# Kernel tuning notes

Hardware: AMD Instinct MI355X
Metric: run time of the kernel (lower is better)

The kernel has to match this reference:

```python
import jax, jax.numpy as jnp
import numpy as np

B, S, E, H, A = 2, 1024, 1024, 16, 3
HD = E // H

def setup_inputs() -> dict:
    key = jax.random.key(0)
    ks = jax.random.split(key, 8)
    return {
        "query": jax.random.normal(ks[0], (B, S, E), dtype=jnp.float32),
        "key": jax.random.normal(ks[1], (B, S, E), dtype=jnp.float32),
        "value": jax.random.normal(ks[2], (B, S, E), dtype=jnp.float32),
        "aid": jax.random.normal(ks[3], (B, S, S, A), dtype=jnp.float32),
        "mixer_w": jax.random.uniform(ks[4], (H, A + 1, 1), dtype=jnp.float32),
        "mixer_b": jax.random.uniform(ks[5], (H, 1), dtype=jnp.float32),
        "Wo": jax.random.normal(ks[6], (E, E), dtype=jnp.float32) * 0.02,
        "bo": jax.random.normal(ks[7], (E,), dtype=jnp.float32) * 0.02,
        "aid_scale": jnp.array([0.1], dtype=jnp.float32),
    }

def reference(query, key, value, aid, mixer_w, mixer_b, Wo, bo, aid_scale):
    scale = HD ** -0.5
    # Faithful to source: raw row-major reshape (B,S,E)->(B,H,S,HD)
    q = query.reshape(B, H, S, HD)
    k = key.reshape(B, H, S, HD)
    v = value.reshape(B, H, S, HD)
    attn = jnp.einsum('bhqd,bhkd->bhqk', q, k) * scale  # (B,H,S,S)
    aid_h = jnp.broadcast_to(aid[:, None], (B, H, S, S, A))
    mix_in = jnp.concatenate([attn[..., None], aid_h], axis=-1)  # (B,H,S,S,A+1)
    mixed = jnp.einsum('bhqki,hio->bhqko', mix_in, mixer_w) + mixer_b[None, :, None, None, :]
    mixed = jax.nn.relu(mixed)[..., 0]  # (B,H,S,S)
    attn = attn + mixed * aid_scale[0]
    pre_softmax_attn = attn
    attn = jax.nn.softmax(attn, axis=-1)
    out = jnp.einsum('bhqk,bhkd->bhqd', attn, v)
    out = out.transpose(0, 2, 1, 3).reshape(B, S, E)
    out = out @ Wo.T + bo
    return out, attn, pre_softmax_attn
```

## Files before the change

kernel.cpp:

```cpp
#include <hip/hip_runtime.h>
#include <hip/hip_bf16.h>

using u16 = unsigned short;
typedef __attribute__((ext_vector_type(8))) short short8;
typedef __attribute__((ext_vector_type(4))) float f32x4;

constexpr int Bc = 2, Sc = 1024, Ec = 1024, Hc = 16, HDc = 64;
constexpr float SCALE = 0.125f;

__device__ __forceinline__ u16 f2bf(float f) {
    union { float f; unsigned u; } v{f};
    unsigned r = v.u + 0x7FFF + ((v.u >> 16) & 1);
    return (u16)(r >> 16);
}
__device__ __forceinline__ float bf2f(u16 x) {
    union { unsigned u; float f; } v; v.u = ((unsigned)x) << 16; return v.f;
}

__global__ __launch_bounds__(256) void k_prep(
    const float* __restrict__ Q, const float* __restrict__ K,
    const float* __restrict__ Wo, const float* __restrict__ V,
    u16* __restrict__ Qb, u16* __restrict__ Kb, u16* __restrict__ Wob,
    u16* __restrict__ Vt)
{
    __shared__ float tile[64][65];
    const int bid = blockIdx.x;
    const int tid = threadIdx.x;

    if (bid < 2560) {
        const float* src; u16* dst; int base;
        if (bid < 1024)      { src = Q;  dst = Qb;  base = bid; }
        else if (bid < 2048) { src = K;  dst = Kb;  base = bid - 1024; }
        else                 { src = Wo; dst = Wob; base = bid - 2048; }
        const int i = (base * 256 + tid) * 8;
        float4 a = *(const float4*)&src[i];
        float4 b = *(const float4*)&src[i + 4];
        u16 t[8] = {f2bf(a.x), f2bf(a.y), f2bf(a.z), f2bf(a.w),
                    f2bf(b.x), f2bf(b.y), f2bf(b.z), f2bf(b.w)};
        *(short8*)&dst[i] = *(short8*)t;
        return;
    }

    const int bx = bid - 2560;
    const int bh = bx >> 4;
    const int k0 = (bx & 15) * 64;
    const float* Vp = V + (size_t)bh * Sc * HDc + (size_t)k0 * HDc;

    #pragma unroll
    for (int it = 0; it < 4; ++it) {
        int idx = tid + it * 256;
        int k = idx >> 4, d4 = idx & 15;
        float4 v = *(const float4*)&Vp[k * HDc + d4 * 4];
        tile[d4 * 4 + 0][k] = v.x;
        tile[d4 * 4 + 1][k] = v.y;
        tile[d4 * 4 + 2][k] = v.z;
        tile[d4 * 4 + 3][k] = v.w;
    }
    __syncthreads();

    u16* Op = Vt + (size_t)bh * HDc * Sc + k0;
    #pragma unroll
    for (int it = 0; it < 4; ++it) {
        int idx = tid + it * 256;
        int d = idx >> 4, kq = idx & 15;
        u16 t[4];
        #pragma unroll
        for (int j = 0; j < 4; ++j) t[j] = f2bf(tile[d][kq * 4 + j]);
        *(uint2*)&Op[(size_t)d * Sc + kq * 4] = *(uint2*)t;
    }
}

__global__ __launch_bounds__(256, 2) void k_scores(
    const u16* __restrict__ Qb, const u16* __restrict__ Kb,
    const float* __restrict__ aid, const float* __restrict__ mw,
    const float* __restrict__ mb, const float* __restrict__ ascale,
    float* __restrict__ pre)
{
    __shared__ u16 Qs[64 * 64];
    __shared__ u16 Ks[64 * 64];

    const int bid = blockIdx.x;
    const int kt = bid & 15;
    const int qt = (bid >> 4) & 15;
    const int b  = bid >> 8;

    const int tid = threadIdx.x;
    const int w = tid >> 6, lane = tid & 63;
    const int lrow = lane & 15, lhi = lane >> 4;

    float a3[4][4][3];
    #pragma unroll
    for (int r = 0; r < 4; ++r) {
        const size_t qg = (size_t)(b * Sc + qt * 64 + w * 16 + lhi * 4 + r) * Sc;
        #pragma unroll
        for (int fk = 0; fk < 4; ++fk) {
            const float* ap = aid + (qg + kt * 64 + fk * 16 + lrow) * 3;
            float2 t2 = *(const float2*)ap;
            a3[r][fk][0] = t2.x; a3[r][fk][1] = t2.y; a3[r][fk][2] = ap[2];
        }
    }

    const float asc = ascale[0];
    const u16* Qbase = Qb + ((size_t)b * Hc * Sc + qt * 64) * HDc;
    const u16* Kbase = Kb + ((size_t)b * Hc * Sc + kt * 64) * HDc;

    const int r0 = tid >> 3,          g0 = tid & 7;
    const int r1 = (tid + 256) >> 3,  g1 = tid & 7;
    const int gs0 = (g0 ^ (r0 & 7)) * 8;
    const int gs1 = (g1 ^ (r1 & 7)) * 8;

    short8 qp0, qp1, kp0, kp1;
    {
        qp0 = *(const short8*)&Qbase[r0 * 64 + g0 * 8];
        qp1 = *(const short8*)&Qbase[r1 * 64 + g1 * 8];
        kp0 = *(const short8*)&Kbase[r0 * 64 + g0 * 8];
        kp1 = *(const short8*)&Kbase[r1 * 64 + g1 * 8];
    }

    for (int h = 0; h < Hc; ++h) {
        *(short8*)&Qs[r0 * 64 + gs0] = qp0;
        *(short8*)&Qs[r1 * 64 + gs1] = qp1;
        *(short8*)&Ks[r0 * 64 + gs0] = kp0;
        *(short8*)&Ks[r1 * 64 + gs1] = kp1;
        __syncthreads();

        if (h < Hc - 1) {
            const u16* Qp = Qbase + (size_t)(h + 1) * Sc * HDc;
            const u16* Kp = Kbase + (size_t)(h + 1) * Sc * HDc;
            qp0 = *(const short8*)&Qp[r0 * 64 + g0 * 8];
            qp1 = *(const short8*)&Qp[r1 * 64 + g1 * 8];
            kp0 = *(const short8*)&Kp[r0 * 64 + g0 * 8];
            kp1 = *(const short8*)&Kp[r1 * 64 + g1 * 8];
        }

        f32x4 acc[4] = {};
        #pragma unroll
        for (int ks2 = 0; ks2 < 2; ++ks2) {
            const int rq = w * 16 + lrow;
            short8 af = *(const short8*)&Qs[rq * 64 + ((ks2 * 4 + lhi) ^ (rq & 7)) * 8];
            #pragma unroll
            for (int fk = 0; fk < 4; ++fk) {
                const int rk = fk * 16 + lrow;
                short8 bf = *(const short8*)&Ks[rk * 64 + ((ks2 * 4 + lhi) ^ (rk & 7)) * 8];
                acc[fk] = __builtin_amdgcn_mfma_f32_16x16x32_bf16(af, bf, acc[fk], 0, 0, 0);
            }
        }

        const float w0 = mw[h * 4 + 0], w1 = mw[h * 4 + 1];
        const float w2 = mw[h * 4 + 2], w3 = mw[h * 4 + 3];
        const float bias = mb[h];
        float* prow0 = pre + ((size_t)(b * Hc + h) * Sc + qt * 64 + w * 16 + lhi * 4) * Sc
                     + kt * 64 + lrow;
        #pragma unroll
        for (int r = 0; r < 4; ++r) {
            #pragma unroll
            for (int fk = 0; fk < 4; ++fk) {
                float s = acc[fk][r] * SCALE;
                float mm = s * w0 + a3[r][fk][0] * w1 + a3[r][fk][1] * w2
                         + a3[r][fk][2] * w3 + bias;
                prow0[(size_t)r * Sc + fk * 16] = s + fmaxf(mm, 0.f) * asc;
            }
        }
        __syncthreads();
    }
}

__global__ __launch_bounds__(512, 4) void k_spv(
    const float* __restrict__ pre, const u16* __restrict__ Vt,
    float* __restrict__ attn, u16* __restrict__ Omid)
{
    __shared__ u16 band[32 * 1024];
    __shared__ float s_m[32];
    __shared__ float s_lp[4][32];

    const int bid = blockIdx.x;
    const int bh  = bid >> 5;
    const int qt  = (bid & 31) * 32;
    const int b   = bh >> 4, h = bh & 15;

    const int tid  = threadIdx.x;
    const int w    = tid >> 6, lane = tid & 63;
    const int lrow = lane & 15, lhi = lane >> 4;

    const int arow = tid >> 4;
    const int s16  = tid & 15;
    const int g    = s16 & 7;
    const int kh   = s16 >> 3;
    const int asw  = arow & 7;
    const float* prow = pre + ((size_t)bh * Sc + qt + arow) * Sc;
    float m = -1e30f;
    #pragma unroll
    for (int k2 = 0; k2 < 8; ++k2) {
        const int kt = kh * 8 + k2;
        const float* p0 = prow + kt * 64 + g * 8;
        float s[8];
        *(float4*)&s[0] = *(const float4*)p0;
        *(float4*)&s[4] = *(const float4*)(p0 + 4);
        u16 t[8];
        #pragma unroll
        for (int j = 0; j < 8; ++j) { m = fmaxf(m, s[j]); t[j] = f2bf(s[j]); }
        *(short8*)&band[arow * 1024 + (kt * 8 + (g ^ asw)) * 8] = *(short8*)t;
    }
    m = fmaxf(m, __shfl_xor(m, 1));
    m = fmaxf(m, __shfl_xor(m, 2));
    m = fmaxf(m, __shfl_xor(m, 4));
    m = fmaxf(m, __shfl_xor(m, 8));
    if (s16 == 0) s_m[arow] = m;
    __syncthreads();

    const int rf = w & 1, kf = w >> 1;
    const int brow = rf * 16 + lrow;
    const int bsw  = brow & 7;
    const float mreg = s_m[brow];
    const u16* Vbase = Vt + (size_t)bh * HDc * Sc;
    float l = 0.f;
    f32x4 acc[4] = {};

    #pragma unroll
    for (int j = 0; j < 4; ++j) {
        const int kt = kf * 4 + j;
        const int soA = brow * 1024 + (kt * 8 + (lhi ^ bsw)) * 8;
        const int soB = brow * 1024 + (kt * 8 + ((lhi + 4) ^ bsw)) * 8;
        short8 ra = *(const short8*)&band[soA];
        short8 rb = *(const short8*)&band[soB];
        u16 ea[8], eb[8];
        #pragma unroll
        for (int jj = 0; jj < 8; ++jj) {
            float va = __expf(bf2f((u16)ra[jj]) - mreg); l += va; ea[jj] = f2bf(va);
            float vb = __expf(bf2f((u16)rb[jj]) - mreg); l += vb; eb[jj] = f2bf(vb);
        }
        *(short8*)&band[soA] = *(short8*)ea;
        *(short8*)&band[soB] = *(short8*)eb;
        short8 A0 = *(short8*)ea, A1 = *(short8*)eb;
        #pragma unroll
        for (int fd = 0; fd < 4; ++fd) {
            const u16* vp = Vbase + (size_t)(fd * 16 + lrow) * Sc + kt * 64;
            short8 b0 = *(const short8*)&vp[lhi * 8];
            short8 b1 = *(const short8*)&vp[(lhi + 4) * 8];
            acc[fd] = __builtin_amdgcn_mfma_f32_16x16x32_bf16(A0, b0, acc[fd], 0, 0, 0);
            acc[fd] = __builtin_amdgcn_mfma_f32_16x16x32_bf16(A1, b1, acc[fd], 0, 0, 0);
        }
    }
    l += __shfl_xor(l, 16);
    l += __shfl_xor(l, 32);
    if (lhi == 0) s_lp[kf][brow] = l;
    __syncthreads();

    const float lt = s_lp[0][arow] + s_lp[1][arow] + s_lp[2][arow] + s_lp[3][arow];
    const float inv = 1.f / lt;
    float* arowp = attn + ((size_t)bh * Sc + qt + arow) * Sc;
    #pragma unroll
    for (int k2 = 0; k2 < 8; ++k2) {
        const int kt = kh * 8 + k2;
        short8 ra = *(const short8*)&band[arow * 1024 + (kt * 8 + (g ^ asw)) * 8];
        float o[8];
        #pragma unroll
        for (int jj = 0; jj < 8; ++jj) o[jj] = bf2f((u16)ra[jj]) * inv;
        *(float4*)&arowp[kt * 64 + g * 8]     = *(float4*)&o[0];
        *(float4*)&arowp[kt * 64 + g * 8 + 4] = *(float4*)&o[4];
    }
    __syncthreads();

    float* ovl = (float*)band;
    #pragma unroll
    for (int reg = 0; reg < 4; ++reg) {
        const int rowO = rf * 16 + lhi * 4 + reg;
        #pragma unroll
        for (int fd = 0; fd < 4; ++fd)
            ovl[(kf * 32 + rowO) * 68 + fd * 16 + lrow] = acc[fd][reg];
    }
    __syncthreads();

    const int orow_ = tid >> 4;
    const int dq    = tid & 15;
    const float lr = 1.f / (s_lp[0][orow_] + s_lp[1][orow_]
                          + s_lp[2][orow_] + s_lp[3][orow_]);
    u16 t4[4];
    #pragma unroll
    for (int dd = 0; dd < 4; ++dd) {
        const int d = dq * 4 + dd;
        float v = ovl[(0 * 32 + orow_) * 68 + d] + ovl[(1 * 32 + orow_) * 68 + d]
                + ovl[(2 * 32 + orow_) * 68 + d] + ovl[(3 * 32 + orow_) * 68 + d];
        t4[dd] = f2bf(v * lr);
    }
    *(uint2*)&Omid[((size_t)b * Sc + qt + orow_) * Ec + h * HDc + dq * 4] = *(uint2*)t4;
}

__global__ __launch_bounds__(256, 2) void k_proj(
    const u16* __restrict__ Ob, const u16* __restrict__ Wob,
    const float* __restrict__ bo, float* __restrict__ out)
{
    __shared__ u16 Xs[128 * 64];
    __shared__ u16 Ws[64 * 64];

    const int bid = blockIdx.x;
    const int mt = (bid >> 4) * 128;
    const int et = (bid & 15) * 64;

    const int tid = threadIdx.x;
    const int w = tid >> 6, lane = tid & 63;
    const int lrow = lane & 15, lhi = lane >> 4;

    f32x4 acc[2][4] = {};

    for (int kb = 0; kb < Ec; kb += 64) {
        #pragma unroll
        for (int it = 0; it < 4; ++it) {
            int idx = tid + it * 256;
            int r = idx >> 3, g = idx & 7;
            *(short8*)&Xs[r * 64 + (g ^ (r & 7)) * 8] =
                *(const short8*)&Ob[(size_t)(mt + r) * Ec + kb + g * 8];
        }
        #pragma unroll
        for (int it = 0; it < 2; ++it) {
            int idx = tid + it * 256;
            int r = idx >> 3, g = idx & 7;
            *(short8*)&Ws[r * 64 + (g ^ (r & 7)) * 8] =
                *(const short8*)&Wob[(size_t)(et + r) * Ec + kb + g * 8];
        }
        __syncthreads();

        #pragma unroll
        for (int ks = 0; ks < 2; ++ks) {
            short8 af[2], bfr[4];
            int g = ks * 4 + lhi;
            #pragma unroll
            for (int fq = 0; fq < 2; ++fq) {
                int rq = w * 32 + fq * 16 + lrow;
                af[fq] = *(const short8*)&Xs[rq * 64 + (g ^ (rq & 7)) * 8];
            }
            #pragma unroll
            for (int fd = 0; fd < 4; ++fd) {
                int rv = fd * 16 + lrow;
                bfr[fd] = *(const short8*)&Ws[rv * 64 + (g ^ (rv & 7)) * 8];
            }
            #pragma unroll
            for (int fq = 0; fq < 2; ++fq)
                #pragma unroll
                for (int fd = 0; fd < 4; ++fd)
                    acc[fq][fd] = __builtin_amdgcn_mfma_f32_16x16x32_bf16(
                        af[fq], bfr[fd], acc[fq][fd], 0, 0, 0);
        }
        __syncthreads();
    }

    #pragma unroll
    for (int fq = 0; fq < 2; ++fq)
        #pragma unroll
        for (int r = 0; r < 4; ++r) {
            const int m = mt + w * 32 + fq * 16 + lhi * 4 + r;
            float* orow = out + (size_t)m * Ec + et;
            #pragma unroll
            for (int fd = 0; fd < 4; ++fd) {
                int e = fd * 16 + lrow;
                orow[e] = acc[fq][fd][r] + bo[et + e];
            }
        }
}

extern "C" void kernel_launch(void* const* d_in, const int* in_sizes, int n_in,
                              void* d_out, int out_size, void* d_ws, size_t ws_size,
                              hipStream_t stream) {
    const float* query  = (const float*)d_in[0];
    const float* key    = (const float*)d_in[1];
    const float* value  = (const float*)d_in[2];
    const float* aid    = (const float*)d_in[3];
    const float* mw     = (const float*)d_in[4];
    const float* mb     = (const float*)d_in[5];
    const float* Wo     = (const float*)d_in[6];
    const float* bo     = (const float*)d_in[7];
    const float* ascale = (const float*)d_in[8];

    float* out_p  = (float*)d_out;
    float* attn_p = out_p + (size_t)Bc * Sc * Ec;
    float* pre_p  = attn_p + (size_t)Bc * Hc * Sc * Sc;

    u16* Vtb  = (u16*)d_ws;
    u16* Omid = Vtb  + (size_t)2 * 1024 * 1024;
    u16* Qb   = Omid + (size_t)2 * 1024 * 1024;
    u16* Kb   = Qb   + (size_t)2 * 1024 * 1024;
    u16* Wob  = Kb   + (size_t)2 * 1024 * 1024;

    k_prep<<<3072, 256, 0, stream>>>(query, key, Wo, value, Qb, Kb, Wob, Vtb);
    k_scores<<<Bc * 16 * 16, 256, 0, stream>>>(Qb, Kb, aid, mw, mb, ascale, pre_p);
    k_spv<<<Bc * Hc * (Sc / 32), 512, 0, stream>>>(pre_p, Vtb, attn_p, Omid);
    k_proj<<<(Bc * Sc / 128) * (Ec / 64), 256, 0, stream>>>(Omid, Wob, bo, out_p);
}
```

Before: 141.9 us.

## Fuse score computation into softmax-PV kernel to avoid re-reading pre-softmax scores

Merges the QK^T score/mixer kernel into the softmax·V kernel. Each block now computes its 32-row score band with MFMA directly from global Q/K, writes pre-softmax to global, and also stores a bf16 copy into shared memory. This removes the global re-read of the full pre-softmax tensor and one kernel launch. In exchange, aid is read once per head instead of being shared across all 16 heads, K is loaded from global without LDS staging, and the bf16 LDS stores are scalar and scattered.

```diff
diff --git a/kernel.cpp b/kernel.cpp
--- a/kernel.cpp
+++ b/kernel.cpp
@@ -70,107 +70,15 @@
     }
 }
 
-__global__ __launch_bounds__(256, 2) void k_scores(
+__global__ __launch_bounds__(512, 4) void k_fused(
     const u16* __restrict__ Qb, const u16* __restrict__ Kb,
     const float* __restrict__ aid, const float* __restrict__ mw,
     const float* __restrict__ mb, const float* __restrict__ ascale,
-    float* __restrict__ pre)
-{
-    __shared__ u16 Qs[64 * 64];
-    __shared__ u16 Ks[64 * 64];
-
-    const int bid = blockIdx.x;
-    const int kt = bid & 15;
-    const int qt = (bid >> 4) & 15;
-    const int b  = bid >> 8;
-
-    const int tid = threadIdx.x;
-    const int w = tid >> 6, lane = tid & 63;
-    const int lrow = lane & 15, lhi = lane >> 4;
-
-    float a3[4][4][3];
-    #pragma unroll
-    for (int r = 0; r < 4; ++r) {
-        const size_t qg = (size_t)(b * Sc + qt * 64 + w * 16 + lhi * 4 + r) * Sc;
-        #pragma unroll
-        for (int fk = 0; fk < 4; ++fk) {
-            const float* ap = aid + (qg + kt * 64 + fk * 16 + lrow) * 3;
-            float2 t2 = *(const float2*)ap;
-            a3[r][fk][0] = t2.x; a3[r][fk][1] = t2.y; a3[r][fk][2] = ap[2];
-        }
-    }
-
-    const float asc = ascale[0];
-    const u16* Qbase = Qb + ((size_t)b * Hc * Sc + qt * 64) * HDc;
-    const u16* Kbase = Kb + ((size_t)b * Hc * Sc + kt * 64) * HDc;
-
-    const int r0 = tid >> 3,          g0 = tid & 7;
-    const int r1 = (tid + 256) >> 3,  g1 = tid & 7;
-    const int gs0 = (g0 ^ (r0 & 7)) * 8;
-    const int gs1 = (g1 ^ (r1 & 7)) * 8;
-
-    short8 qp0, qp1, kp0, kp1;
-    {
-        qp0 = *(const short8*)&Qbase[r0 * 64 + g0 * 8];
-        qp1 = *(const short8*)&Qbase[r1 * 64 + g1 * 8];
-        kp0 = *(const short8*)&Kbase[r0 * 64 + g0 * 8];
-        kp1 = *(const short8*)&Kbase[r1 * 64 + g1 * 8];
-    }
-
-    for (int h = 0; h < Hc; ++h) {
-        *(short8*)&Qs[r0 * 64 + gs0] = qp0;
-        *(short8*)&Qs[r1 * 64 + gs1] = qp1;
-        *(short8*)&Ks[r0 * 64 + gs0] = kp0;
-        *(short8*)&Ks[r1 * 64 + gs1] = kp1;
-        __syncthreads();
-
-        if (h < Hc - 1) {
-            const u16* Qp = Qbase + (size_t)(h + 1) * Sc * HDc;
-            const u16* Kp = Kbase + (size_t)(h + 1) * Sc * HDc;
-            qp0 = *(const short8*)&Qp[r0 * 64 + g0 * 8];
-            qp1 = *(const short8*)&Qp[r1 * 64 + g1 * 8];
-            kp0 = *(const short8*)&Kp[r0 * 64 + g0 * 8];
-            kp1 = *(const short8*)&Kp[r1 * 64 + g1 * 8];
-        }
-
-        f32x4 acc[4] = {};
-        #pragma unroll
-        for (int ks2 = 0; ks2 < 2; ++ks2) {
-            const int rq = w * 16 + lrow;
-            short8 af = *(const short8*)&Qs[rq * 64 + ((ks2 * 4 + lhi) ^ (rq & 7)) * 8];
-            #pragma unroll
-            for (int fk = 0; fk < 4; ++fk) {
-                const int rk = fk * 16 + lrow;
-                short8 bf = *(const short8*)&Ks[rk * 64 + ((ks2 * 4 + lhi) ^ (rk & 7)) * 8];
-                acc[fk] = __builtin_amdgcn_mfma_f32_16x16x32_bf16(af, bf, acc[fk], 0, 0, 0);
-            }
-        }
-
-        const float w0 = mw[h * 4 + 0], w1 = mw[h * 4 + 1];
-        const float w2 = mw[h * 4 + 2], w3 = mw[h * 4 + 3];
-        const float bias = mb[h];
-        float* prow0 = pre + ((size_t)(b * Hc + h) * Sc + qt * 64 + w * 16 + lhi * 4) * Sc
-                     + kt * 64 + lrow;
-        #pragma unroll
-        for (int r = 0; r < 4; ++r) {
-            #pragma unroll
-            for (int fk = 0; fk < 4; ++fk) {
-                float s = acc[fk][r] * SCALE;
-                float mm = s * w0 + a3[r][fk][0] * w1 + a3[r][fk][1] * w2
-                         + a3[r][fk][2] * w3 + bias;
-                prow0[(size_t)r * Sc + fk * 16] = s + fmaxf(mm, 0.f) * asc;
-            }
-        }
-        __syncthreads();
-    }
-}
-
-__global__ __launch_bounds__(512, 4) void k_spv(
-    const float* __restrict__ pre, const u16* __restrict__ Vt,
+    const u16* __restrict__ Vt, float* __restrict__ pre,
     float* __restrict__ attn, u16* __restrict__ Omid)
 {
     __shared__ u16 band[32 * 1024];
-    __shared__ float s_m[32];
+    __shared__ float s_mp[4][32];
     __shared__ float s_lp[4][32];
 
     const int bid = blockIdx.x;
@@ -181,37 +89,71 @@
     const int tid  = threadIdx.x;
     const int w    = tid >> 6, lane = tid & 63;
     const int lrow = lane & 15, lhi = lane >> 4;
-
-    const int arow = tid >> 4;
-    const int s16  = tid & 15;
-    const int g    = s16 & 7;
-    const int kh   = s16 >> 3;
-    const int asw  = arow & 7;
-    const float* prow = pre + ((size_t)bh * Sc + qt + arow) * Sc;
-    float m = -1e30f;
-    #pragma unroll
-    for (int k2 = 0; k2 < 8; ++k2) {
-        const int kt = kh * 8 + k2;
-        const float* p0 = prow + kt * 64 + g * 8;
-        float s[8];
-        *(float4*)&s[0] = *(const float4*)p0;
-        *(float4*)&s[4] = *(const float4*)(p0 + 4);
-        u16 t[8];
-        #pragma unroll
-        for (int j = 0; j < 8; ++j) { m = fmaxf(m, s[j]); t[j] = f2bf(s[j]); }
-        *(short8*)&band[arow * 1024 + (kt * 8 + (g ^ asw)) * 8] = *(short8*)t;
-    }
-    m = fmaxf(m, __shfl_xor(m, 1));
-    m = fmaxf(m, __shfl_xor(m, 2));
-    m = fmaxf(m, __shfl_xor(m, 4));
-    m = fmaxf(m, __shfl_xor(m, 8));
-    if (s16 == 0) s_m[arow] = m;
-    __syncthreads();
-
     const int rf = w & 1, kf = w >> 1;
+
+    const float w0 = mw[h * 4 + 0], w1 = mw[h * 4 + 1];
+    const float w2 = mw[h * 4 + 2], w3 = mw[h * 4 + 3];
+    const float bias = mb[h];
+    const float asc  = ascale[0];
+
+    const u16* Qp = Qb + ((size_t)(b * Hc + h) * Sc + qt + rf * 16 + lrow) * HDc;
+    short8 aq0 = *(const short8*)&Qp[lhi * 8];
+    short8 aq1 = *(const short8*)&Qp[32 + lhi * 8];
+    const u16* Kp = Kb + (size_t)(b * Hc + h) * Sc * HDc;
+
+    float pm[4] = {-1e30f, -1e30f, -1e30f, -1e30f};
+    const int qrow_base = qt + rf * 16 + lhi * 4;
+
+    #pragma unroll
+    for (int j = 0; j < 4; ++j) {
+        const int kt = kf * 4 + j;
+        f32x4 accs[4] = {};
+        #pragma unroll
+        for (int fk = 0; fk < 4; ++fk) {
+            const u16* kp = Kp + (size_t)(kt * 64 + fk * 16 + lrow) * HDc;
+            short8 b0 = *(const short8*)&kp[lhi * 8];
+            short8 b1 = *(const short8*)&kp[32 + lhi * 8];
+            accs[fk] = __builtin_amdgcn_mfma_f32_16x16x32_bf16(aq0, b0, accs[fk], 0, 0, 0);
+            accs[fk] = __builtin_amdgcn_mfma_f32_16x16x32_bf16(aq1, b1, accs[fk], 0, 0, 0);
+        }
+        #pragma unroll
+        for (int r = 0; r < 4; ++r) {
+            const int qrow = qrow_base + r;
+            const float* ap = aid + ((size_t)(b * Sc + qrow) * Sc + kt * 64 + lrow) * 3;
+            float* prow = pre + ((size_t)(b * Hc + h) * Sc + qrow) * Sc + kt * 64 + lrow;
+            const int row = rf * 16 + lhi * 4 + r;
+            const int rsw = row & 7;
+            #pragma unroll
+            for (int fk = 0; fk < 4; ++fk) {
+                float2 t2 = *(const float2*)&ap[fk * 48];
+                float a2 = ap[fk * 48 + 2];
+                float s = accs[fk][r] * SCALE;
+                float mm = s * w0 + t2.x * w1 + t2.y * w2 + a2 * w3 + bias;
+                float pv = s + fmaxf(mm, 0.f) * asc;
+                pm[r] = fmaxf(pm[r], pv);
+                prow[fk * 16] = pv;
+                const int col = fk * 16 + lrow;
+                band[row * 1024 + (kt * 8 + ((col >> 3) ^ rsw)) * 8 + (col & 7)] = f2bf(pv);
+            }
+        }
+    }
+    #pragma unroll
+    for (int r = 0; r < 4; ++r) {
+        pm[r] = fmaxf(pm[r], __shfl_xor(pm[r], 1));
+        pm[r] = fmaxf(pm[r], __shfl_xor(pm[r], 2));
+        pm[r] = fmaxf(pm[r], __shfl_xor(pm[r], 4));
+        pm[r] = fmaxf(pm[r], __shfl_xor(pm[r], 8));
+    }
+    if (lrow == 0) {
+        #pragma unroll
+        for (int r = 0; r < 4; ++r) s_mp[kf][rf * 16 + lhi * 4 + r] = pm[r];
+    }
+    __syncthreads();
+
     const int brow = rf * 16 + lrow;
     const int bsw  = brow & 7;
-    const float mreg = s_m[brow];
+    const float mreg = fmaxf(fmaxf(s_mp[0][brow], s_mp[1][brow]),
+                             fmaxf(s_mp[2][brow], s_mp[3][brow]));
     const u16* Vbase = Vt + (size_t)bh * HDc * Sc;
     float l = 0.f;
     f32x4 acc[4] = {};
@@ -246,6 +188,11 @@
     if (lhi == 0) s_lp[kf][brow] = l;
     __syncthreads();
 
+    const int arow = tid >> 4;
+    const int s16  = tid & 15;
+    const int g    = s16 & 7;
+    const int kh   = s16 >> 3;
+    const int asw  = arow & 7;
     const float lt = s_lp[0][arow] + s_lp[1][arow] + s_lp[2][arow] + s_lp[3][arow];
     const float inv = 1.f / lt;
     float* arowp = attn + ((size_t)bh * Sc + qt + arow) * Sc;
@@ -382,7 +329,7 @@
     u16* Wob  = Kb   + (size_t)2 * 1024 * 1024;
 
     k_prep<<<3072, 256, 0, stream>>>(query, key, Wo, value, Qb, Kb, Wob, Vtb);
-    k_scores<<<Bc * 16 * 16, 256, 0, stream>>>(Qb, Kb, aid, mw, mb, ascale, pre_p);
-    k_spv<<<Bc * Hc * (Sc / 32), 512, 0, stream>>>(pre_p, Vtb, attn_p, Omid);
+    k_fused<<<Bc * Hc * (Sc / 32), 512, 0, stream>>>(
+        Qb, Kb, aid, mw, mb, ascale, Vtb, pre_p, attn_p, Omid);
     k_proj<<<(Bc * Sc / 128) * (Ec / 64), 256, 0, stream>>>(Omid, Wob, bo, out_p);
 }
```

Result: no change. 143.6 us (+1.2%).
